# Performance work log

Hardware: AMD Instinct MI355X
Metric: run time of the kernel (lower is better)

The kernel has to match this reference:

```python
import jax, jax.numpy as jnp
import numpy as np

EDGE_TEXT_IMG = 2
D_MODEL = 256
N_HEADS = 8
N_LAYERS = 3
INPUT_DIM = 768
LN_EPS = 1e-5
CONFLICT_EPS = 1e-6


def setup_inputs() -> dict:
    key = jax.random.key(0)
    ks = jax.random.split(key, 32)
    B, N, E = 16, 512, 4096
    d, H, L = D_MODEL, N_HEADS, N_LAYERS
    s = 0.02
    inp = {
        'node_feats': jax.random.normal(ks[0], (B, N, INPUT_DIM), jnp.float32),
        'node_mask': jnp.ones((B, N), bool),
        'text_mask': jax.random.randint(ks[1], (B, N), 0, 2).astype(bool),
        'image_mask': jax.random.randint(ks[2], (B, N), 0, 2).astype(bool),
        'global_indices': jax.random.randint(ks[3], (B,), 0, N),
        'edge_index': jax.random.randint(ks[4], (B, 2, E), 0, N),
        'edge_type': jax.random.randint(ks[5], (B, E), 0, 4),
        'edge_weight': jax.random.uniform(ks[6], (B, E), jnp.float32),
        # params
        'W_in': jax.random.normal(ks[7], (INPUT_DIM, d)) * s,
        'b_in': jnp.zeros((d,)),
        'Wqkv': jax.random.normal(ks[8], (L, d, 3 * d)) * s,
        'bqkv': jnp.zeros((L, 3 * d)),
        'Wo': jax.random.normal(ks[9], (L, d, d)) * s,
        'bo': jnp.zeros((L, d)),
        'ln1_g': jnp.ones((L, d)), 'ln1_b': jnp.zeros((L, d)),
        'ln2_g': jnp.ones((L, d)), 'ln2_b': jnp.zeros((L, d)),
        'Wff1': jax.random.normal(ks[10], (L, d, 4 * d)) * s,
        'bff1': jnp.zeros((L, 4 * d)),
        'Wff2': jax.random.normal(ks[11], (L, 4 * d, d)) * s,
        'bff2': jnp.zeros((L, d)),
        'et_emb': jax.random.normal(ks[12], (4, H)) * s,
        'Wm1': jax.random.normal(ks[13], (3 * d + 1, 2 * d)) * s,
        'bm1': jnp.zeros((2 * d,)),
        'Wm2': jax.random.normal(ks[14], (2 * d, d)) * s,
        'bm2': jnp.zeros((d,)),
        'Wm3': jax.random.normal(ks[15], (d, 1)) * s,
        'bm3': jnp.zeros((1,)),
    }
    return inp


def _ln(x, g, b):
    mu = jnp.mean(x, -1, keepdims=True)
    var = jnp.mean((x - mu) ** 2, -1, keepdims=True)
    return (x - mu) * jax.lax.rsqrt(var + LN_EPS) * g + b


def _build_bias(edge_index, edge_type, edge_weight, et_emb, N):
    # vectorized scatter-add of per-edge head biases into dense [B,H,N,N]
    B = edge_index.shape[0]
    src, dst = edge_index[:, 0], edge_index[:, 1]  # [B,E]
    vals = et_emb[edge_type]  # [B,E,H]
    vals = vals + jnp.where(edge_type == EDGE_TEXT_IMG, edge_weight, 0.0)[..., None]
    bias = jnp.zeros((B, N, N, et_emb.shape[1]), vals.dtype)
    bias = bias.at[jnp.arange(B)[:, None], src, dst].add(vals)
    return bias.transpose(0, 3, 1, 2)  # [B,H,N,N]


def _forward(node_feats, node_mask, text_mask, image_mask, global_indices,
             edge_index, edge_type, edge_weight,
             W_in, b_in, Wqkv, bqkv, Wo, bo, ln1_g, ln1_b, ln2_g, ln2_b,
             Wff1, bff1, Wff2, bff2, et_emb, Wm1, bm1, Wm2, bm2, Wm3, bm3):
    B, N, _ = node_feats.shape
    H = N_HEADS
    hd = D_MODEL // H
    attn_bias = _build_bias(edge_index, edge_type, edge_weight, et_emb, N)
    x = node_feats @ W_in + b_in  # [B,N,d]
    key_mask = node_mask[:, None, None, :]  # [B,1,1,N]
    for l in range(N_LAYERS):
        qkv = x @ Wqkv[l] + bqkv[l]
        qkv = qkv.reshape(B, N, 3, H, hd).transpose(2, 0, 3, 1, 4)
        q, k, v = qkv[0], qkv[1], qkv[2]  # [B,H,N,hd]
        scores = jnp.einsum('bhnd,bhmd->bhnm', q, k) / np.sqrt(hd).astype(np.float32)
        scores = scores + attn_bias
        scores = jnp.where(key_mask, scores, -jnp.inf)
        attn = jax.nn.softmax(scores, axis=-1)
        out = jnp.einsum('bhnm,bhmd->bhnd', attn, v)
        out = out.transpose(0, 2, 1, 3).reshape(B, N, D_MODEL)
        out = out @ Wo[l] + bo[l]
        x = _ln(x + out, ln1_g[l], ln1_b[l])
        ff = jax.nn.gelu(x @ Wff1[l] + bff1[l], approximate=False) @ Wff2[l] + bff2[l]
        x = _ln(x + ff, ln2_g[l], ln2_b[l])
    tm = text_mask.astype(x.dtype)
    im = image_mask.astype(x.dtype)
    tc = jnp.clip(tm.sum(1, keepdims=True), 1.0)
    ic = jnp.clip(im.sum(1, keepdims=True), 1.0)
    text_pool = (x * tm[..., None]).sum(1) / tc
    image_pool = (x * im[..., None]).sum(1) / ic
    global_embeds = x[jnp.arange(B), global_indices]
    n1 = jnp.maximum(jnp.linalg.norm(text_pool, axis=-1), CONFLICT_EPS)
    n2 = jnp.maximum(jnp.linalg.norm(image_pool, axis=-1), CONFLICT_EPS)
    cos = jnp.sum(text_pool * image_pool, -1) / (n1 * n2)
    conflict = (1.0 - cos)[:, None]
    combined = jnp.concatenate([global_embeds, text_pool, image_pool, conflict], -1)
    h = jax.nn.gelu(combined @ Wm1 + bm1, approximate=False)
    h = jax.nn.gelu(h @ Wm2 + bm2, approximate=False)
    logits = (h @ Wm3 + bm3)[:, 0]
    return logits


def reference(node_feats, node_mask, text_mask, image_mask, global_indices,
              edge_index, edge_type, edge_weight,
              W_in, b_in, Wqkv, bqkv, Wo, bo, ln1_g, ln1_b, ln2_g, ln2_b,
              Wff1, bff1, Wff2, bff2, et_emb, Wm1, bm1, Wm2, bm2, Wm3, bm3):
    return _forward(node_feats, node_mask, text_mask, image_mask, global_indices,
                    edge_index, edge_type, edge_weight,
                    W_in, b_in, Wqkv, bqkv, Wo, bo, ln1_g, ln1_b, ln2_g, ln2_b,
                    Wff1, bff1, Wff2, bff2, et_emb, Wm1, bm1, Wm2, bm2, Wm3, bm3)
```

## Files before the change

kernel.cpp:

```cpp
#include <hip/hip_runtime.h>
#include <hip/hip_bf16.h>
#include <math.h>

#define Bb 16
#define Nn 512
#define Dd 256
#define Hh 8
#define HD 32
#define Ll 3
#define INDIM 768
#define Ee 4096
#define FF 1024
#define KP2 72
#define NBUCK 32768

typedef unsigned short u16;
typedef __bf16 bf16x8 __attribute__((ext_vector_type(8)));
typedef float f32x4 __attribute__((ext_vector_type(4)));
typedef u16 us8 __attribute__((ext_vector_type(8)));
typedef u16 us4 __attribute__((ext_vector_type(4)));

__device__ __forceinline__ float gelu_exact(float x) {
    return 0.5f * x * (1.0f + erff(x * 0.70710678118654752f));
}

__device__ __forceinline__ u16 f2bf(float x) {
    union { __bf16 b; u16 u; } cv;
    cv.b = (__bf16)x;
    return cv.u;
}
__device__ __forceinline__ float bf2f(u16 h) {
    return __uint_as_float(((unsigned int)h) << 16);
}

__device__ __forceinline__ int ebucket(int b, int src, int dst) {
    return ((b * 32 + (src >> 4)) * 4 + (dst >> 7)) * 16 + (src & 15);
}


__global__ __launch_bounds__(256) void zero2_kernel(int* __restrict__ a, int na,
                                                    int* __restrict__ b, int nb) {
    int gid = blockIdx.x * 256 + threadIdx.x;
    if (gid < na) a[gid] = 0;
    else {
        int j = gid - na;
        if (j < nb) b[j] = 0;
    }
}

__global__ __launch_bounds__(256) void count_kernel(const int* __restrict__ edge_index,
                                                    int* __restrict__ counts) {
    int gid = blockIdx.x * 256 + threadIdx.x;
    int b = gid >> 12;
    int e = gid & (Ee - 1);
    int src = edge_index[b * 2 * Ee + e];
    int dst = edge_index[b * 2 * Ee + Ee + e];
    atomicAdd(&counts[ebucket(b, src, dst)], 1);
}

__global__ __launch_bounds__(1024) void scan_kernel(const int* __restrict__ counts,
                                                    int* __restrict__ offsets,
                                                    int* __restrict__ cursor) {
    __shared__ int ssum[1024];
    int t = threadIdx.x;
    int local[32];
    int s = 0;
#pragma unroll
    for (int i = 0; i < 32; i++) { local[i] = counts[t * 32 + i]; s += local[i]; }
    ssum[t] = s;
    __syncthreads();
    for (int off = 1; off < 1024; off *= 2) {
        __syncthreads();
        int v = (t >= off) ? ssum[t - off] : 0;
        __syncthreads();
        ssum[t] += v;
    }
    __syncthreads();
    int base = (t > 0) ? ssum[t - 1] : 0;
#pragma unroll
    for (int i = 0; i < 32; i++) {
        offsets[t * 32 + i] = base;
        cursor[t * 32 + i] = base;
        base += local[i];
    }
    if (t == 1023) offsets[NBUCK] = base;
}

__global__ __launch_bounds__(256) void scatter_kernel(const int* __restrict__ edge_index,
                                                      const int* __restrict__ edge_type,
                                                      const float* __restrict__ edge_weight,
                                                      int* __restrict__ cursor,
                                                      int2* __restrict__ pelist) {
    int gid = blockIdx.x * 256 + threadIdx.x;
    int b = gid >> 12;
    int e = gid & (Ee - 1);
    int src = edge_index[b * 2 * Ee + e];
    int dst = edge_index[b * 2 * Ee + Ee + e];
    int ty = edge_type[b * Ee + e];
    float wgt = edge_weight[b * Ee + e];
    int pos = atomicAdd(&cursor[ebucket(b, src, dst)], 1);
    int2 pe;
    pe.x = (src << 20) | (dst << 4) | ty;
    pe.y = __float_as_int(wgt);
    pelist[pos] = pe;
}


__global__ __launch_bounds__(256) void wsplit(const float* __restrict__ W,
                                              u16* __restrict__ Wh,
                                              u16* __restrict__ Wl,
                                              int K, int N) {
    size_t moff = (size_t)blockIdx.z * K * N;
    const float* Ws = W + moff;
    u16* Whs = Wh + moff;
    u16* Wls = Wl + moff;
    int n = blockIdx.x * 256 + threadIdx.x;
    int k0 = blockIdx.y * 8;
    float w[8];
#pragma unroll
    for (int i = 0; i < 8; i++) w[i] = Ws[(size_t)(k0 + i) * N + n];
    u16 h[8], l[8];
#pragma unroll
    for (int i = 0; i < 8; i++) {
        h[i] = f2bf(w[i]);
        l[i] = f2bf(w[i] - bf2f(h[i]));
    }
    us8 hv = {h[0], h[1], h[2], h[3], h[4], h[5], h[6], h[7]};
    us8 lv = {l[0], l[1], l[2], l[3], l[4], l[5], l[6], l[7]};
    *(us8*)&Whs[(size_t)n * K + k0] = hv;
    *(us8*)&Wls[(size_t)n * K + k0] = lv;
}


__global__ __launch_bounds__(256) void gemm_mfma64(const float* __restrict__ A,
                                                   const u16* __restrict__ Bh,
                                                   const u16* __restrict__ Bl,
                                                   const float* __restrict__ bias,
                                                   float* __restrict__ C,
                                                   int M, int K, int N, int act) {
    __shared__ u16 sAh[64 * KP2];
    __shared__ u16 sAl[64 * KP2];
    __shared__ u16 sBh[64 * KP2];
    __shared__ u16 sBl[64 * KP2];

    int t = threadIdx.x;
    int w = t >> 6, L = t & 63;
    int wr = w >> 1, wc = w & 1;
    int lane15 = L & 15, quad = L >> 4;
    int row0 = blockIdx.y * 64, col0 = blockIdx.x * 64;

    f32x4 acc[2][2];
#pragma unroll
    for (int mi = 0; mi < 2; mi++)
#pragma unroll
        for (int ni = 0; ni < 2; ni++) acc[mi][ni] = {0.f, 0.f, 0.f, 0.f};

    int ar0 = t >> 3, ak0 = (t & 7) * 8;
    int bn0 = t >> 2, bk0 = (t & 3) * 16;

    const float* Ap0 = &A[(size_t)(row0 + ar0) * K + ak0];
    const float* Ap1 = &A[(size_t)(row0 + ar0 + 32) * K + ak0];
    const u16* Bhp = &Bh[(size_t)(col0 + bn0) * K + bk0];
    const u16* Blp = &Bl[(size_t)(col0 + bn0) * K + bk0];

    float4 av0[2], av1[2];
    us8 bhv[2], blv[2];
#pragma unroll
    for (int j = 0; j < 2; j++) {
        av0[j] = *(const float4*)&Ap0[4 * j];
        av1[j] = *(const float4*)&Ap1[4 * j];
        bhv[j] = *(const us8*)&Bhp[8 * j];
        blv[j] = *(const us8*)&Blp[8 * j];
    }

    for (int k0 = 0; k0 < K; k0 += 64) {
        __syncthreads();
#pragma unroll
        for (int j = 0; j < 2; j++) {
            {
                float a[4] = {av0[j].x, av0[j].y, av0[j].z, av0[j].w};
                u16 h[4], l[4];
#pragma unroll
                for (int i = 0; i < 4; i++) { h[i] = f2bf(a[i]); l[i] = f2bf(a[i] - bf2f(h[i])); }
                us4 hv = {h[0], h[1], h[2], h[3]};
                us4 lv = {l[0], l[1], l[2], l[3]};
                *(us4*)&sAh[ar0 * KP2 + ak0 + 4 * j] = hv;
                *(us4*)&sAl[ar0 * KP2 + ak0 + 4 * j] = lv;
            }
            {
                float a[4] = {av1[j].x, av1[j].y, av1[j].z, av1[j].w};
                u16 h[4], l[4];
#pragma unroll
                for (int i = 0; i < 4; i++) { h[i] = f2bf(a[i]); l[i] = f2bf(a[i] - bf2f(h[i])); }
                us4 hv = {h[0], h[1], h[2], h[3]};
                us4 lv = {l[0], l[1], l[2], l[3]};
                *(us4*)&sAh[(ar0 + 32) * KP2 + ak0 + 4 * j] = hv;
                *(us4*)&sAl[(ar0 + 32) * KP2 + ak0 + 4 * j] = lv;
            }
            *(us8*)&sBh[bn0 * KP2 + bk0 + 8 * j] = bhv[j];
            *(us8*)&sBl[bn0 * KP2 + bk0 + 8 * j] = blv[j];
        }
        __syncthreads();

        if (k0 + 64 < K) {
#pragma unroll
            for (int j = 0; j < 2; j++) {
                av0[j] = *(const float4*)&Ap0[k0 + 64 + 4 * j];
                av1[j] = *(const float4*)&Ap1[k0 + 64 + 4 * j];
                bhv[j] = *(const us8*)&Bhp[k0 + 64 + 8 * j];
                blv[j] = *(const us8*)&Blp[k0 + 64 + 8 * j];
            }
        }

#pragma unroll
        for (int half = 0; half < 2; half++) {
            int kofs = half * 32 + quad * 8;
            us8 ahr[2], alr[2], bhr[2], blr[2];
#pragma unroll
            for (int mi = 0; mi < 2; mi++) {
                int ro = (wr * 32 + mi * 16 + lane15) * KP2 + kofs;
                ahr[mi] = *(const us8*)&sAh[ro];
                alr[mi] = *(const us8*)&sAl[ro];
            }
#pragma unroll
            for (int ni = 0; ni < 2; ni++) {
                int ro = (wc * 32 + ni * 16 + lane15) * KP2 + kofs;
                bhr[ni] = *(const us8*)&sBh[ro];
                blr[ni] = *(const us8*)&sBl[ro];
            }
#pragma unroll
            for (int mi = 0; mi < 2; mi++) {
                bf16x8 ah = *(const bf16x8*)&ahr[mi];
                bf16x8 al = *(const bf16x8*)&alr[mi];
#pragma unroll
                for (int ni = 0; ni < 2; ni++) {
                    bf16x8 bh = *(const bf16x8*)&bhr[ni];
                    bf16x8 bl = *(const bf16x8*)&blr[ni];
                    acc[mi][ni] = __builtin_amdgcn_mfma_f32_16x16x32_bf16(ah, bh, acc[mi][ni], 0, 0, 0);
                    acc[mi][ni] = __builtin_amdgcn_mfma_f32_16x16x32_bf16(ah, bl, acc[mi][ni], 0, 0, 0);
                    acc[mi][ni] = __builtin_amdgcn_mfma_f32_16x16x32_bf16(al, bh, acc[mi][ni], 0, 0, 0);
                }
            }
        }
    }

#pragma unroll
    for (int mi = 0; mi < 2; mi++) {
#pragma unroll
        for (int ni = 0; ni < 2; ni++) {
            int col = col0 + wc * 32 + ni * 16 + lane15;
            float bcol = bias[col];
#pragma unroll
            for (int r = 0; r < 4; r++) {
                int row = row0 + wr * 32 + mi * 16 + quad * 4 + r;
                float u = acc[mi][ni][r] + bcol;
                if (act == 1) u = gelu_exact(u);
                C[(size_t)row * N + col] = u;
            }
        }
    }
}


__global__ __launch_bounds__(256) void gemm_mfma128(const float* __restrict__ A,
                                                    const u16* __restrict__ Bh,
                                                    const u16* __restrict__ Bl,
                                                    const float* __restrict__ bias,
                                                    float* __restrict__ C,
                                                    int M, int K, int N, int act) {
    __shared__ u16 sAh[128 * KP2];
    __shared__ u16 sAl[128 * KP2];
    __shared__ u16 sBh[128 * KP2];
    __shared__ u16 sBl[128 * KP2];

    int t = threadIdx.x;
    int w = t >> 6, L = t & 63;
    int wr = w >> 1, wc = w & 1;
    int lane15 = L & 15, quad = L >> 4;
    int row0 = blockIdx.y * 128, col0 = blockIdx.x * 128;

    f32x4 acc[4][4];
#pragma unroll
    for (int mi = 0; mi < 4; mi++)
#pragma unroll
        for (int ni = 0; ni < 4; ni++) acc[mi][ni] = {0.f, 0.f, 0.f, 0.f};

    int ar0 = t >> 3, ak0 = (t & 7) * 8;
    int bn0 = t >> 2, bk0 = (t & 3) * 16;

    const float* Ap = &A[(size_t)(row0 + ar0) * K + ak0];
    const u16* Bhp = &Bh[(size_t)(col0 + bn0) * K + bk0];
    const u16* Blp = &Bl[(size_t)(col0 + bn0) * K + bk0];

    float4 av[4][2];
    us8 bhv[2][2], blv[2][2];
#pragma unroll
    for (int i = 0; i < 4; i++)
#pragma unroll
        for (int j = 0; j < 2; j++) av[i][j] = *(const float4*)&Ap[(size_t)(32 * i) * K + 4 * j];
#pragma unroll
    for (int i = 0; i < 2; i++)
#pragma unroll
        for (int j = 0; j < 2; j++) {
            bhv[i][j] = *(const us8*)&Bhp[(size_t)(64 * i) * K + 8 * j];
            blv[i][j] = *(const us8*)&Blp[(size_t)(64 * i) * K + 8 * j];
        }

    for (int k0 = 0; k0 < K; k0 += 64) {
        __syncthreads();
#pragma unroll
        for (int i = 0; i < 4; i++)
#pragma unroll
            for (int j = 0; j < 2; j++) {
                float a[4] = {av[i][j].x, av[i][j].y, av[i][j].z, av[i][j].w};
                u16 h[4], l[4];
#pragma unroll
                for (int q = 0; q < 4; q++) { h[q] = f2bf(a[q]); l[q] = f2bf(a[q] - bf2f(h[q])); }
                us4 hv = {h[0], h[1], h[2], h[3]};
                us4 lv = {l[0], l[1], l[2], l[3]};
                *(us4*)&sAh[(ar0 + 32 * i) * KP2 + ak0 + 4 * j] = hv;
                *(us4*)&sAl[(ar0 + 32 * i) * KP2 + ak0 + 4 * j] = lv;
            }
#pragma unroll
        for (int i = 0; i < 2; i++)
#pragma unroll
            for (int j = 0; j < 2; j++) {
                *(us8*)&sBh[(bn0 + 64 * i) * KP2 + bk0 + 8 * j] = bhv[i][j];
                *(us8*)&sBl[(bn0 + 64 * i) * KP2 + bk0 + 8 * j] = blv[i][j];
            }
        __syncthreads();

        if (k0 + 64 < K) {
#pragma unroll
            for (int i = 0; i < 4; i++)
#pragma unroll
                for (int j = 0; j < 2; j++)
                    av[i][j] = *(const float4*)&Ap[(size_t)(32 * i) * K + k0 + 64 + 4 * j];
#pragma unroll
            for (int i = 0; i < 2; i++)
#pragma unroll
                for (int j = 0; j < 2; j++) {
                    bhv[i][j] = *(const us8*)&Bhp[(size_t)(64 * i) * K + k0 + 64 + 8 * j];
                    blv[i][j] = *(const us8*)&Blp[(size_t)(64 * i) * K + k0 + 64 + 8 * j];
                }
        }

#pragma unroll
        for (int half = 0; half < 2; half++) {
            int kofs = half * 32 + quad * 8;
            us8 ahr[4], alr[4], bhr[4], blr[4];
#pragma unroll
            for (int mi = 0; mi < 4; mi++) {
                int ro = (wr * 64 + mi * 16 + lane15) * KP2 + kofs;
                ahr[mi] = *(const us8*)&sAh[ro];
                alr[mi] = *(const us8*)&sAl[ro];
            }
#pragma unroll
            for (int ni = 0; ni < 4; ni++) {
                int ro = (wc * 64 + ni * 16 + lane15) * KP2 + kofs;
                bhr[ni] = *(const us8*)&sBh[ro];
                blr[ni] = *(const us8*)&sBl[ro];
            }
#pragma unroll
            for (int mi = 0; mi < 4; mi++) {
                bf16x8 ah = *(const bf16x8*)&ahr[mi];
                bf16x8 al = *(const bf16x8*)&alr[mi];
#pragma unroll
                for (int ni = 0; ni < 4; ni++) {
                    bf16x8 bh = *(const bf16x8*)&bhr[ni];
                    bf16x8 bl = *(const bf16x8*)&blr[ni];
                    acc[mi][ni] = __builtin_amdgcn_mfma_f32_16x16x32_bf16(ah, bh, acc[mi][ni], 0, 0, 0);
                    acc[mi][ni] = __builtin_amdgcn_mfma_f32_16x16x32_bf16(ah, bl, acc[mi][ni], 0, 0, 0);
                    acc[mi][ni] = __builtin_amdgcn_mfma_f32_16x16x32_bf16(al, bh, acc[mi][ni], 0, 0, 0);
                }
            }
        }
    }

#pragma unroll
    for (int mi = 0; mi < 4; mi++) {
#pragma unroll
        for (int ni = 0; ni < 4; ni++) {
            int col = col0 + wc * 64 + ni * 16 + lane15;
            float bcol = bias[col];
#pragma unroll
            for (int r = 0; r < 4; r++) {
                int row = row0 + wr * 64 + mi * 16 + quad * 4 + r;
                float u = acc[mi][ni][r] + bcol;
                if (act == 1) u = gelu_exact(u);
                C[(size_t)row * N + col] = u;
            }
        }
    }
}


#define SBP 132

__global__ __launch_bounds__(256, 2) void attn_kernel(const float* __restrict__ qkv,
                                                      const int* __restrict__ node_mask,
                                                      const int* __restrict__ offsets,
                                                      const int2* __restrict__ pelist,
                                                      const float* __restrict__ et_emb,
                                                      float* __restrict__ outbuf) {
    int bid = blockIdx.x;
    int quarter = bid & 3;
    int h = (bid >> 2) & 7;
    int b = bid >> 5;
    int t = threadIdx.x;
    int w = t >> 6, L = t & 63;
    int quad = L >> 4, lane15 = L & 15;
    int q8 = quad * 8;

    __shared__ u16 sKh[128 * 40];
    __shared__ u16 sKl[128 * 40];
    __shared__ u16 sVh[32 * SBP];
    __shared__ u16 sVl[32 * SBP];
    __shared__ float sS[4 * 16 * SBP];

    float* Sw = &sS[w * 16 * SBP];
    const float scale = 0.17677669529663687f;
    int nbase = quarter * 128 + w * 32;
    int mt0 = t >> 5, dt = t & 31;

    float etl0 = et_emb[0 * Hh + h];
    float etl1 = et_emb[1 * Hh + h];
    float etl2 = et_emb[2 * Hh + h];
    float etl3 = et_emb[3 * Hh + h];

    us8 Qh[2], Ql[2];
#pragma unroll
    for (int sub = 0; sub < 2; sub++) {
        size_t row = (size_t)(b * Nn + nbase + sub * 16 + lane15);
        float4 qa = *(const float4*)&qkv[row * 768 + h * HD + q8];
        float4 qb = *(const float4*)&qkv[row * 768 + h * HD + q8 + 4];
        float qv[8] = {qa.x, qa.y, qa.z, qa.w, qb.x, qb.y, qb.z, qb.w};
#pragma unroll
        for (int j = 0; j < 8; j++) {
            float xq = qv[j] * scale;
            u16 hh = f2bf(xq);
            Qh[sub][j] = hh;
            Ql[sub][j] = f2bf(xq - bf2f(hh));
        }
    }

    float Mst[2] = {-INFINITY, -INFINITY};
    float Lst[2] = {0.0f, 0.0f};
    f32x4 O[2][2];
#pragma unroll
    for (int sub = 0; sub < 2; sub++)
#pragma unroll
        for (int dc = 0; dc < 2; dc++) O[sub][dc] = {0.f, 0.f, 0.f, 0.f};

    float pk[16], pv[16];
#pragma unroll
    for (int j = 0; j < 16; j++) {
        size_t grow = (size_t)(b * Nn + mt0 + 8 * j) * 768 + h * HD + dt;
        pk[j] = qkv[grow + 256];
        pv[j] = qkv[grow + 512];
    }

    for (int T = 0; T < 4; T++) {
        int m0 = T * 128;
        __syncthreads();
#pragma unroll
        for (int j = 0; j < 16; j++) {
            int m = mt0 + 8 * j;
            u16 kh = f2bf(pk[j]);
            sKh[m * 40 + dt] = kh;
            sKl[m * 40 + dt] = f2bf(pk[j] - bf2f(kh));
            u16 vh = f2bf(pv[j]);
            sVh[dt * SBP + m] = vh;
            sVl[dt * SBP + m] = f2bf(pv[j] - bf2f(vh));
        }
        __syncthreads();
        if (T < 3) {
#pragma unroll
            for (int j = 0; j < 16; j++) {
                size_t grow = (size_t)(b * Nn + (T + 1) * 128 + mt0 + 8 * j) * 768 + h * HD + dt;
                pk[j] = qkv[grow + 256];
                pv[j] = qkv[grow + 512];
            }
        }

        float mk[4][8];
#pragma unroll
        for (int c = 0; c < 4; c++) {
            int4 u0 = *(const int4*)&node_mask[b * Nn + m0 + c * 32 + q8];
            int4 u1 = *(const int4*)&node_mask[b * Nn + m0 + c * 32 + q8 + 4];
            mk[c][0] = u0.x ? 0.f : -INFINITY;
            mk[c][1] = u0.y ? 0.f : -INFINITY;
            mk[c][2] = u0.z ? 0.f : -INFINITY;
            mk[c][3] = u0.w ? 0.f : -INFINITY;
            mk[c][4] = u1.x ? 0.f : -INFINITY;
            mk[c][5] = u1.y ? 0.f : -INFINITY;
            mk[c][6] = u1.z ? 0.f : -INFINITY;
            mk[c][7] = u1.w ? 0.f : -INFINITY;
        }

#pragma unroll
        for (int sub = 0; sub < 2; sub++) {
            int nsub = nbase + sub * 16;
            bf16x8 qh = *(const bf16x8*)&Qh[sub];
            bf16x8 ql = *(const bf16x8*)&Ql[sub];

            f32x4 accS[8];
#pragma unroll
            for (int mc = 0; mc < 8; mc++) accS[mc] = {0.f, 0.f, 0.f, 0.f};
#pragma unroll
            for (int mc = 0; mc < 8; mc++) {
                us8 khr = *(const us8*)&sKh[(mc * 16 + lane15) * 40 + q8];
                us8 klr = *(const us8*)&sKl[(mc * 16 + lane15) * 40 + q8];
                bf16x8 kh = *(const bf16x8*)&khr;
                bf16x8 kl = *(const bf16x8*)&klr;
                accS[mc] = __builtin_amdgcn_mfma_f32_16x16x32_bf16(qh, kh, accS[mc], 0, 0, 0);
                accS[mc] = __builtin_amdgcn_mfma_f32_16x16x32_bf16(qh, kl, accS[mc], 0, 0, 0);
                accS[mc] = __builtin_amdgcn_mfma_f32_16x16x32_bf16(ql, kh, accS[mc], 0, 0, 0);
            }
#pragma unroll
            for (int mc = 0; mc < 8; mc++)
#pragma unroll
                for (int r = 0; r < 4; r++)
                    Sw[(quad * 4 + r) * SBP + mc * 16 + lane15] = accS[mc][r];
            asm volatile("s_waitcnt lgkmcnt(0)" ::: "memory");

            int gb = ((b * 32 + (nsub >> 4)) * 4 + T) * 16;
            int beg = offsets[gb];
// ... 81 lines not shown
#pragma unroll
    for (int sub = 0; sub < 2; sub++) {
        float linv = 1.0f / Lst[sub];
        float lD[4];
#pragma unroll
        for (int r = 0; r < 4; r++) lD[r] = __shfl(linv, (L & 48) | (quad * 4 + r));
#pragma unroll
        for (int dc = 0; dc < 2; dc++)
#pragma unroll
            for (int r = 0; r < 4; r++) {
                int row = nbase + sub * 16 + quad * 4 + r;
                outbuf[(size_t)(b * Nn + row) * Dd + h * HD + dc * 16 + lane15] =
                    O[sub][dc][r] * lD[r];
            }
    }
}


__global__ __launch_bounds__(256) void ln_kernel(float* __restrict__ x,
                                                 const float* __restrict__ res,
                                                 const float* __restrict__ g,
                                                 const float* __restrict__ bta) {
    int row = blockIdx.x * 4 + (threadIdx.x >> 6);
    int L = threadIdx.x & 63;
    size_t base = (size_t)row * Dd + L * 4;
    float4 v4 = *(const float4*)&x[base];
    float4 r4 = *(const float4*)&res[base];
    float v0 = v4.x + r4.x, v1 = v4.y + r4.y, v2 = v4.z + r4.z, v3 = v4.w + r4.w;
    float sm = v0 + v1 + v2 + v3;
#pragma unroll
    for (int o = 32; o > 0; o >>= 1) sm += __shfl_xor(sm, o);
    float mu = sm * (1.0f / Dd);
    float d0 = v0 - mu, d1 = v1 - mu, d2 = v2 - mu, d3 = v3 - mu;
    float s2 = d0 * d0 + d1 * d1 + d2 * d2 + d3 * d3;
#pragma unroll
    for (int o = 32; o > 0; o >>= 1) s2 += __shfl_xor(s2, o);
    float rsig = 1.0f / sqrtf(s2 * (1.0f / Dd) + 1e-5f);
    float4 g4 = *(const float4*)&g[L * 4];
    float4 b4 = *(const float4*)&bta[L * 4];
    float4 o4;
    o4.x = d0 * rsig * g4.x + b4.x;
    o4.y = d1 * rsig * g4.y + b4.y;
    o4.z = d2 * rsig * g4.z + b4.z;
    o4.w = d3 * rsig * g4.w + b4.w;
    *(float4*)&x[base] = o4;
}


__global__ __launch_bounds__(256) void pool_kernel(const float* __restrict__ x,
                                                   const int* __restrict__ text_mask,
                                                   const int* __restrict__ image_mask,
                                                   float* __restrict__ pools) {
    int b = blockIdx.y;
    int n0 = blockIdx.x * 32;
    int t = threadIdx.x;
    float tp = 0.0f, ip = 0.0f, c1 = 0.0f, c2 = 0.0f;
    for (int n = n0; n < n0 + 32; n++) {
        float xv = x[(size_t)(b * Nn + n) * Dd + t];
        int tm = text_mask[b * Nn + n];
        int im = image_mask[b * Nn + n];
        tp += tm ? xv : 0.0f;
        ip += im ? xv : 0.0f;
        c1 += (float)tm;
        c2 += (float)im;
    }
    atomicAdd(&pools[b * 514 + t], tp);
    atomicAdd(&pools[b * 514 + 256 + t], ip);
    if (t == 0) {
        atomicAdd(&pools[b * 514 + 512], c1);
        atomicAdd(&pools[b * 514 + 513], c2);
    }
}

__global__ __launch_bounds__(256) void comb_kernel(const float* __restrict__ x,
                                                   const float* __restrict__ pools,
                                                   const int* __restrict__ gidx,
                                                   float* __restrict__ comb) {
    int b = blockIdx.x;
    int t = threadIdx.x;
    __shared__ float redd[12];
    float tc = fmaxf(pools[b * 514 + 512], 1.0f);
    float ic = fmaxf(pools[b * 514 + 513], 1.0f);
    float tp = pools[b * 514 + t] / tc;
    float ip = pools[b * 514 + 256 + t] / ic;
    int gi = gidx[b];
    comb[b * 776 + t] = x[(size_t)(b * Nn + gi) * Dd + t];
    comb[b * 776 + 256 + t] = tp;
    comb[b * 776 + 512 + t] = ip;
    float dotv = tp * ip, n1v = tp * tp, n2v = ip * ip;
    for (int o = 32; o > 0; o >>= 1) {
        dotv += __shfl_down(dotv, o);
        n1v += __shfl_down(n1v, o);
        n2v += __shfl_down(n2v, o);
    }
    if ((t & 63) == 0) { redd[t >> 6] = dotv; redd[4 + (t >> 6)] = n1v; redd[8 + (t >> 6)] = n2v; }
    __syncthreads();
    if (t == 0) {
        float dd = redd[0] + redd[1] + redd[2] + redd[3];
        float a1 = fmaxf(sqrtf(redd[4] + redd[5] + redd[6] + redd[7]), 1e-6f);
        float a2 = fmaxf(sqrtf(redd[8] + redd[9] + redd[10] + redd[11]), 1e-6f);
        comb[b * 776 + 768] = 1.0f - dd / (a1 * a2);
    }
}

__global__ __launch_bounds__(256) void h1_kernel(const float* __restrict__ comb,
                                                 const float* __restrict__ Wm1,
                                                 const float* __restrict__ bm1,
                                                 float* __restrict__ h1) {
    int b = blockIdx.y;
    int jc = blockIdx.x;
    int t = threadIdx.x;
    __shared__ float scomb[776];
    __shared__ float partial[2][128];
    for (int i = t; i < 769; i += 256) scomb[i] = comb[b * 776 + i];
    __syncthreads();
    int j = jc * 128 + (t & 127);
    int kh = t >> 7;
    int kbeg = kh ? 384 : 0;
    int kend = kh ? 769 : 384;
    float acc = 0.0f;
#pragma unroll 8
    for (int k = kbeg; k < kend; k++) acc += scomb[k] * Wm1[k * 512 + j];
    partial[kh][t & 127] = acc;
    __syncthreads();
    if (t < 128) {
        float v = partial[0][t] + partial[1][t] + bm1[jc * 128 + t];
        h1[b * 512 + jc * 128 + t] = gelu_exact(v);
    }
}

__global__ __launch_bounds__(256) void head_fin(const float* __restrict__ h1,
                                                const float* __restrict__ Wm2,
                                                const float* __restrict__ bm2,
                                                const float* __restrict__ Wm3,
                                                const float* __restrict__ bm3,
                                                float* __restrict__ out) {
    int b = blockIdx.x;
    int t = threadIdx.x;
    __shared__ float h1s[512];
    __shared__ float red[4];
    for (int i = t; i < 512; i += 256) h1s[i] = h1[b * 512 + i];
    __syncthreads();
    float acc = bm2[t];
#pragma unroll 8
    for (int k = 0; k < 512; k++) acc += h1s[k] * Wm2[k * 256 + t];
    float h2 = gelu_exact(acc);
    float lv = h2 * Wm3[t];
    for (int o = 32; o > 0; o >>= 1) lv += __shfl_down(lv, o);
    if ((t & 63) == 0) red[t >> 6] = lv;
    __syncthreads();
    if (t == 0) out[b] = red[0] + red[1] + red[2] + red[3] + bm3[0];
}


#define OFF_IN  0
#define OFF_QKV 196608
#define OFF_O   786432
#define OFF_F1  983040
#define OFF_F2  1769472
#define W_TOTAL 2555904

extern "C" void kernel_launch(void* const* d_in, const int* in_sizes, int n_in,
                              void* d_out, int out_size, void* d_ws, size_t ws_size,
                              hipStream_t stream) {
    const float* node_feats = (const float*)d_in[0];
    const int* node_mask = (const int*)d_in[1];
    const int* text_mask = (const int*)d_in[2];
    const int* image_mask = (const int*)d_in[3];
    const int* gidx = (const int*)d_in[4];
    const int* edge_index = (const int*)d_in[5];
    const int* edge_type = (const int*)d_in[6];
    const float* edge_weight = (const float*)d_in[7];
    const float* W_in = (const float*)d_in[8];
    const float* b_in = (const float*)d_in[9];
    const float* Wqkv = (const float*)d_in[10];
    const float* bqkv = (const float*)d_in[11];
    const float* Wo = (const float*)d_in[12];
    const float* bo = (const float*)d_in[13];
    const float* ln1_g = (const float*)d_in[14];
    const float* ln1_b = (const float*)d_in[15];
    const float* ln2_g = (const float*)d_in[16];
    const float* ln2_b = (const float*)d_in[17];
    const float* Wff1 = (const float*)d_in[18];
    const float* bff1 = (const float*)d_in[19];
    const float* Wff2 = (const float*)d_in[20];
    const float* bff2 = (const float*)d_in[21];
    const float* et_emb = (const float*)d_in[22];
    const float* Wm1 = (const float*)d_in[23];
    const float* bm1 = (const float*)d_in[24];
    const float* Wm2 = (const float*)d_in[25];
    const float* bm2 = (const float*)d_in[26];
    const float* Wm3 = (const float*)d_in[27];
    const float* bm3 = (const float*)d_in[28];

    const int M = Bb * Nn;
    char* ws = (char*)d_ws;
    size_t off = 0;
    auto alloc = [&](size_t bytes) {
        void* p = ws + off;
        off += (bytes + 255) & ~(size_t)255;
        return p;
    };
    float* x = (float*)alloc((size_t)M * Dd * 4);
    float* qkvb = (float*)alloc((size_t)M * FF * 4);
    float* ffb = qkvb;
    float* attnout = (float*)alloc((size_t)M * Dd * 4);
    float* projb = (float*)alloc((size_t)M * Dd * 4);
    int* counts = (int*)alloc((size_t)NBUCK * 4);
    int* offsets = (int*)alloc((size_t)(NBUCK + 1) * 4);
    int* cursor = (int*)alloc((size_t)NBUCK * 4);
    int2* pelist = (int2*)alloc((size_t)Bb * Ee * 8);
    float* pools = (float*)alloc((size_t)Bb * 514 * 4);
    float* comb = (float*)alloc((size_t)Bb * 776 * 4);
    float* h1 = (float*)alloc((size_t)Bb * 512 * 4);
    u16* wh = (u16*)alloc((size_t)W_TOTAL * 2);
    u16* wl = (u16*)alloc((size_t)W_TOTAL * 2);
    (void)ws_size;

    zero2_kernel<<<(NBUCK + Bb * 514 + 255) / 256, 256, 0, stream>>>(
        counts, NBUCK, (int*)pools, Bb * 514);
    count_kernel<<<256, 256, 0, stream>>>(edge_index, counts);
    scan_kernel<<<1, 1024, 0, stream>>>(counts, offsets, cursor);
    scatter_kernel<<<256, 256, 0, stream>>>(edge_index, edge_type, edge_weight, cursor, pelist);

    wsplit<<<dim3(1, 96, 1), 256, 0, stream>>>(W_in, wh + OFF_IN, wl + OFF_IN, 768, 256);
    wsplit<<<dim3(3, 32, 3), 256, 0, stream>>>(Wqkv, wh + OFF_QKV, wl + OFF_QKV, 256, 768);
    wsplit<<<dim3(1, 32, 3), 256, 0, stream>>>(Wo, wh + OFF_O, wl + OFF_O, 256, 256);
    wsplit<<<dim3(4, 32, 3), 256, 0, stream>>>(Wff1, wh + OFF_F1, wl + OFF_F1, 256, 1024);
    wsplit<<<dim3(1, 128, 3), 256, 0, stream>>>(Wff2, wh + OFF_F2, wl + OFF_F2, 1024, 256);

    gemm_mfma64<<<dim3(Dd / 64, M / 64), 256, 0, stream>>>(
        node_feats, wh + OFF_IN, wl + OFF_IN, b_in, x, M, INDIM, Dd, 0);

    for (int l = 0; l < Ll; l++) {
        gemm_mfma128<<<dim3(768 / 128, M / 128), 256, 0, stream>>>(
            x, wh + OFF_QKV + (size_t)l * 196608, wl + OFF_QKV + (size_t)l * 196608,
            bqkv + l * 768, qkvb, M, Dd, 768, 0);
        attn_kernel<<<Bb * Hh * 4, 256, 0, stream>>>(
            qkvb, node_mask, offsets, pelist, et_emb, attnout);
        gemm_mfma64<<<dim3(Dd / 64, M / 64), 256, 0, stream>>>(
            attnout, wh + OFF_O + (size_t)l * 65536, wl + OFF_O + (size_t)l * 65536,
            bo + l * Dd, projb, M, Dd, Dd, 0);
        ln_kernel<<<M / 4, 256, 0, stream>>>(x, projb, ln1_g + l * Dd, ln1_b + l * Dd);
        gemm_mfma128<<<dim3(FF / 128, M / 128), 256, 0, stream>>>(
            x, wh + OFF_F1 + (size_t)l * 262144, wl + OFF_F1 + (size_t)l * 262144,
            bff1 + l * FF, ffb, M, Dd, FF, 1);
        gemm_mfma64<<<dim3(Dd / 64, M / 64), 256, 0, stream>>>(
            ffb, wh + OFF_F2 + (size_t)l * 262144, wl + OFF_F2 + (size_t)l * 262144,
            bff2 + l * Dd, projb, M, FF, Dd, 0);
        ln_kernel<<<M / 4, 256, 0, stream>>>(x, projb, ln2_g + l * Dd, ln2_b + l * Dd);
    }

    pool_kernel<<<dim3(16, Bb), 256, 0, stream>>>(x, text_mask, image_mask, pools);
    comb_kernel<<<Bb, 256, 0, stream>>>(x, pools, gidx, comb);
    h1_kernel<<<dim3(4, Bb), 256, 0, stream>>>(comb, Wm1, bm1, h1);
    head_fin<<<Bb, 256, 0, stream>>>(h1, Wm2, bm2, Wm3, bm3, (float*)d_out);
}
```

Before: 620.4 us.

## Double-buffer GEMM shared memory with smaller K tiles and merge weight-split launches

Both MFMA GEMM kernels now use a K tile of 32 instead of 64 and two shared-memory buffers. This removes one barrier per iteration and lets stores for the next tile overlap the MFMA work on the current one. Launch bounds now request two blocks per CU to raise occupancy. The five weight hi/lo split kernels are merged into one launch to cut launch overhead. In exchange, each K step does less work, so there are more loop iterations, and the row padding of 36 elements may change LDS bank-conflict behaviour.

```diff
diff --git a/kernel.cpp b/kernel.cpp
--- a/kernel.cpp
+++ b/kernel.cpp
@@ -11,7 +11,7 @@
 #define INDIM 768
 #define Ee 4096
 #define FF 1024
-#define KP2 72
+#define KP3 36
 #define NBUCK 32768
 
 typedef unsigned short u16;
@@ -106,19 +106,57 @@
 }
 
 
-__global__ __launch_bounds__(256) void wsplit(const float* __restrict__ W,
-                                              u16* __restrict__ Wh,
-                                              u16* __restrict__ Wl,
-                                              int K, int N) {
-    size_t moff = (size_t)blockIdx.z * K * N;
-    const float* Ws = W + moff;
-    u16* Whs = Wh + moff;
-    u16* Wls = Wl + moff;
-    int n = blockIdx.x * 256 + threadIdx.x;
-    int k0 = blockIdx.y * 8;
+#define OFF_IN  0
+#define OFF_QKV 196608
+#define OFF_O   786432
+#define OFF_F1  983040
+#define OFF_F2  1769472
+#define W_TOTAL 2555904
+
+__global__ __launch_bounds__(256) void wsplit_all(const float* __restrict__ W_in,
+                                                  const float* __restrict__ Wqkv,
+                                                  const float* __restrict__ Wo,
+                                                  const float* __restrict__ Wff1,
+                                                  const float* __restrict__ Wff2,
+                                                  u16* __restrict__ wh,
+                                                  u16* __restrict__ wl) {
+    int bid = blockIdx.x;
+    const float* W;
+    u16 *Wh, *Wl;
+    int K, N, nb, kb;
+    if (bid < 96) {
+        W = W_in; Wh = wh + OFF_IN; Wl = wl + OFF_IN;
+        K = 768; N = 256; nb = 0; kb = bid;
+    } else if (bid < 384) {
+        int lb = bid - 96; int l = lb / 96; lb -= l * 96;
+        W = Wqkv + (size_t)l * 196608;
+        Wh = wh + OFF_QKV + (size_t)l * 196608;
+        Wl = wl + OFF_QKV + (size_t)l * 196608;
+        K = 256; N = 768; nb = lb % 3; kb = lb / 3;
+    } else if (bid < 480) {
+        int lb = bid - 384; int l = lb / 32; lb -= l * 32;
+        W = Wo + (size_t)l * 65536;
+        Wh = wh + OFF_O + (size_t)l * 65536;
+        Wl = wl + OFF_O + (size_t)l * 65536;
+        K = 256; N = 256; nb = 0; kb = lb;
+    } else if (bid < 864) {
+        int lb = bid - 480; int l = lb / 128; lb -= l * 128;
+        W = Wff1 + (size_t)l * 262144;
+        Wh = wh + OFF_F1 + (size_t)l * 262144;
+        Wl = wl + OFF_F1 + (size_t)l * 262144;
+        K = 256; N = 1024; nb = lb % 4; kb = lb / 4;
+    } else {
+        int lb = bid - 864; int l = lb / 128; lb -= l * 128;
+        W = Wff2 + (size_t)l * 262144;
+        Wh = wh + OFF_F2 + (size_t)l * 262144;
+        Wl = wl + OFF_F2 + (size_t)l * 262144;
+        K = 1024; N = 256; nb = 0; kb = lb;
+    }
+    int n = nb * 256 + threadIdx.x;
+    int k0 = kb * 8;
     float w[8];
 #pragma unroll
-    for (int i = 0; i < 8; i++) w[i] = Ws[(size_t)(k0 + i) * N + n];
+    for (int i = 0; i < 8; i++) w[i] = W[(size_t)(k0 + i) * N + n];
     u16 h[8], l[8];
 #pragma unroll
     for (int i = 0; i < 8; i++) {
@@ -127,21 +165,21 @@
     }
     us8 hv = {h[0], h[1], h[2], h[3], h[4], h[5], h[6], h[7]};
     us8 lv = {l[0], l[1], l[2], l[3], l[4], l[5], l[6], l[7]};
-    *(us8*)&Whs[(size_t)n * K + k0] = hv;
-    *(us8*)&Wls[(size_t)n * K + k0] = lv;
-}
-
-
-__global__ __launch_bounds__(256) void gemm_mfma64(const float* __restrict__ A,
-                                                   const u16* __restrict__ Bh,
-                                                   const u16* __restrict__ Bl,
-                                                   const float* __restrict__ bias,
-                                                   float* __restrict__ C,
-                                                   int M, int K, int N, int act) {
-    __shared__ u16 sAh[64 * KP2];
-    __shared__ u16 sAl[64 * KP2];
-    __shared__ u16 sBh[64 * KP2];
-    __shared__ u16 sBl[64 * KP2];
+    *(us8*)&Wh[(size_t)n * K + k0] = hv;
+    *(us8*)&Wl[(size_t)n * K + k0] = lv;
+}
+
+
+__global__ __launch_bounds__(256, 2) void gemm_mfma64(const float* __restrict__ A,
+                                                      const u16* __restrict__ Bh,
+                                                      const u16* __restrict__ Bl,
+                                                      const float* __restrict__ bias,
+                                                      float* __restrict__ C,
+                                                      int M, int K, int N, int act) {
+    __shared__ u16 sAh[2][64 * KP3];
+    __shared__ u16 sAl[2][64 * KP3];
+    __shared__ u16 sBh[2][64 * KP3];
+    __shared__ u16 sBl[2][64 * KP3];
 
     int t = threadIdx.x;
     int w = t >> 6, L = t & 63;
@@ -155,91 +193,103 @@
 #pragma unroll
         for (int ni = 0; ni < 2; ni++) acc[mi][ni] = {0.f, 0.f, 0.f, 0.f};
 
-    int ar0 = t >> 3, ak0 = (t & 7) * 8;
-    int bn0 = t >> 2, bk0 = (t & 3) * 16;
+    int ar0 = t >> 3, ak0 = (t & 7) * 4;
+    int bn0 = t >> 2, bk0 = (t & 3) * 8;
 
     const float* Ap0 = &A[(size_t)(row0 + ar0) * K + ak0];
     const float* Ap1 = &A[(size_t)(row0 + ar0 + 32) * K + ak0];
     const u16* Bhp = &Bh[(size_t)(col0 + bn0) * K + bk0];
     const u16* Blp = &Bl[(size_t)(col0 + bn0) * K + bk0];
 
-    float4 av0[2], av1[2];
-    us8 bhv[2], blv[2];
-#pragma unroll
-    for (int j = 0; j < 2; j++) {
-        av0[j] = *(const float4*)&Ap0[4 * j];
-        av1[j] = *(const float4*)&Ap1[4 * j];
-        bhv[j] = *(const us8*)&Bhp[8 * j];
-        blv[j] = *(const us8*)&Blp[8 * j];
-    }
-
-    for (int k0 = 0; k0 < K; k0 += 64) {
+    float4 av0, av1;
+    us8 bhv, blv;
+    av0 = *(const float4*)&Ap0[0];
+    av1 = *(const float4*)&Ap1[0];
+    bhv = *(const us8*)&Bhp[0];
+    blv = *(const us8*)&Blp[0];
+
+    int nit = K >> 5;
+
+    {
+        float a0[4] = {av0.x, av0.y, av0.z, av0.w};
+        float a1[4] = {av1.x, av1.y, av1.z, av1.w};
+        u16 h0[4], l0[4], h1[4], l1[4];
+#pragma unroll
+        for (int i = 0; i < 4; i++) {
+            h0[i] = f2bf(a0[i]); l0[i] = f2bf(a0[i] - bf2f(h0[i]));
+            h1[i] = f2bf(a1[i]); l1[i] = f2bf(a1[i] - bf2f(h1[i]));
+        }
+        us4 hv0 = {h0[0], h0[1], h0[2], h0[3]}, lv0 = {l0[0], l0[1], l0[2], l0[3]};
+        us4 hv1 = {h1[0], h1[1], h1[2], h1[3]}, lv1 = {l1[0], l1[1], l1[2], l1[3]};
+        *(us4*)&sAh[0][ar0 * KP3 + ak0] = hv0;
+        *(us4*)&sAl[0][ar0 * KP3 + ak0] = lv0;
+        *(us4*)&sAh[0][(ar0 + 32) * KP3 + ak0] = hv1;
+        *(us4*)&sAl[0][(ar0 + 32) * KP3 + ak0] = lv1;
+        *(us8*)&sBh[0][bn0 * KP3 + bk0] = bhv;
+        *(us8*)&sBl[0][bn0 * KP3 + bk0] = blv;
+    }
+    if (nit > 1) {
+        av0 = *(const float4*)&Ap0[32];
+        av1 = *(const float4*)&Ap1[32];
+        bhv = *(const us8*)&Bhp[32];
+        blv = *(const us8*)&Blp[32];
+    }
+
+    for (int i = 0; i < nit; i++) {
         __syncthreads();
-#pragma unroll
-        for (int j = 0; j < 2; j++) {
-            {
-                float a[4] = {av0[j].x, av0[j].y, av0[j].z, av0[j].w};
-                u16 h[4], l[4];
-#pragma unroll
-                for (int i = 0; i < 4; i++) { h[i] = f2bf(a[i]); l[i] = f2bf(a[i] - bf2f(h[i])); }
-                us4 hv = {h[0], h[1], h[2], h[3]};
-                us4 lv = {l[0], l[1], l[2], l[3]};
-                *(us4*)&sAh[ar0 * KP2 + ak0 + 4 * j] = hv;
-                *(us4*)&sAl[ar0 * KP2 + ak0 + 4 * j] = lv;
-            }
-            {
-                float a[4] = {av1[j].x, av1[j].y, av1[j].z, av1[j].w};
-                u16 h[4], l[4];
-#pragma unroll
-                for (int i = 0; i < 4; i++) { h[i] = f2bf(a[i]); l[i] = f2bf(a[i] - bf2f(h[i])); }
-                us4 hv = {h[0], h[1], h[2], h[3]};
-                us4 lv = {l[0], l[1], l[2], l[3]};
-                *(us4*)&sAh[(ar0 + 32) * KP2 + ak0 + 4 * j] = hv;
-                *(us4*)&sAl[(ar0 + 32) * KP2 + ak0 + 4 * j] = lv;
-            }
-            *(us8*)&sBh[bn0 * KP2 + bk0 + 8 * j] = bhv[j];
-            *(us8*)&sBl[bn0 * KP2 + bk0 + 8 * j] = blv[j];
-        }
-        __syncthreads();
-
-        if (k0 + 64 < K) {
-#pragma unroll
-            for (int j = 0; j < 2; j++) {
-                av0[j] = *(const float4*)&Ap0[k0 + 64 + 4 * j];
-                av1[j] = *(const float4*)&Ap1[k0 + 64 + 4 * j];
-                bhv[j] = *(const us8*)&Bhp[k0 + 64 + 8 * j];
-                blv[j] = *(const us8*)&Blp[k0 + 64 + 8 * j];
-            }
-        }
-
-#pragma unroll
-        for (int half = 0; half < 2; half++) {
-            int kofs = half * 32 + quad * 8;
-            us8 ahr[2], alr[2], bhr[2], blr[2];
-#pragma unroll
-            for (int mi = 0; mi < 2; mi++) {
-                int ro = (wr * 32 + mi * 16 + lane15) * KP2 + kofs;
-                ahr[mi] = *(const us8*)&sAh[ro];
-                alr[mi] = *(const us8*)&sAl[ro];
-            }
+        int cur = i & 1;
+        if (i + 1 < nit) {
+            int nxt = cur ^ 1;
+            float a0[4] = {av0.x, av0.y, av0.z, av0.w};
+            float a1[4] = {av1.x, av1.y, av1.z, av1.w};
+            u16 h0[4], l0[4], h1[4], l1[4];
+#pragma unroll
+            for (int q = 0; q < 4; q++) {
+                h0[q] = f2bf(a0[q]); l0[q] = f2bf(a0[q] - bf2f(h0[q]));
+                h1[q] = f2bf(a1[q]); l1[q] = f2bf(a1[q] - bf2f(h1[q]));
+            }
+            us4 hv0 = {h0[0], h0[1], h0[2], h0[3]}, lv0 = {l0[0], l0[1], l0[2], l0[3]};
+            us4 hv1 = {h1[0], h1[1], h1[2], h1[3]}, lv1 = {l1[0], l1[1], l1[2], l1[3]};
+            *(us4*)&sAh[nxt][ar0 * KP3 + ak0] = hv0;
+            *(us4*)&sAl[nxt][ar0 * KP3 + ak0] = lv0;
+            *(us4*)&sAh[nxt][(ar0 + 32) * KP3 + ak0] = hv1;
+            *(us4*)&sAl[nxt][(ar0 + 32) * KP3 + ak0] = lv1;
+            *(us8*)&sBh[nxt][bn0 * KP3 + bk0] = bhv;
+            *(us8*)&sBl[nxt][bn0 * KP3 + bk0] = blv;
+            if (i + 2 < nit) {
+                int ko = (i + 2) * 32;
+                av0 = *(const float4*)&Ap0[ko];
+                av1 = *(const float4*)&Ap1[ko];
+                bhv = *(const us8*)&Bhp[ko];
+                blv = *(const us8*)&Blp[ko];
+            }
+        }
+
+        int kof = quad * 8;
+        us8 ahr[2], alr[2], bhr[2], blr[2];
+#pragma unroll
+        for (int mi = 0; mi < 2; mi++) {
+            int ro = (wr * 32 + mi * 16 + lane15) * KP3 + kof;
+            ahr[mi] = *(const us8*)&sAh[cur][ro];
+            alr[mi] = *(const us8*)&sAl[cur][ro];
+        }
+#pragma unroll
+        for (int ni = 0; ni < 2; ni++) {
+            int ro = (wc * 32 + ni * 16 + lane15) * KP3 + kof;
+            bhr[ni] = *(const us8*)&sBh[cur][ro];
+            blr[ni] = *(const us8*)&sBl[cur][ro];
+        }
+#pragma unroll
+        for (int mi = 0; mi < 2; mi++) {
+            bf16x8 ah = *(const bf16x8*)&ahr[mi];
+            bf16x8 al = *(const bf16x8*)&alr[mi];
 #pragma unroll
             for (int ni = 0; ni < 2; ni++) {
-                int ro = (wc * 32 + ni * 16 + lane15) * KP2 + kofs;
-                bhr[ni] = *(const us8*)&sBh[ro];
-                blr[ni] = *(const us8*)&sBl[ro];
-            }
-#pragma unroll
-            for (int mi = 0; mi < 2; mi++) {
-                bf16x8 ah = *(const bf16x8*)&ahr[mi];
-                bf16x8 al = *(const bf16x8*)&alr[mi];
-#pragma unroll
-                for (int ni = 0; ni < 2; ni++) {
-                    bf16x8 bh = *(const bf16x8*)&bhr[ni];
-                    bf16x8 bl = *(const bf16x8*)&blr[ni];
-                    acc[mi][ni] = __builtin_amdgcn_mfma_f32_16x16x32_bf16(ah, bh, acc[mi][ni], 0, 0, 0);
-                    acc[mi][ni] = __builtin_amdgcn_mfma_f32_16x16x32_bf16(ah, bl, acc[mi][ni], 0, 0, 0);
-                    acc[mi][ni] = __builtin_amdgcn_mfma_f32_16x16x32_bf16(al, bh, acc[mi][ni], 0, 0, 0);
-                }
+                bf16x8 bh = *(const bf16x8*)&bhr[ni];
+                bf16x8 bl = *(const bf16x8*)&blr[ni];
+                acc[mi][ni] = __builtin_amdgcn_mfma_f32_16x16x32_bf16(ah, bh, acc[mi][ni], 0, 0, 0);
+                acc[mi][ni] = __builtin_amdgcn_mfma_f32_16x16x32_bf16(ah, bl, acc[mi][ni], 0, 0, 0);
+                acc[mi][ni] = __builtin_amdgcn_mfma_f32_16x16x32_bf16(al, bh, acc[mi][ni], 0, 0, 0);
             }
         }
     }
@@ -262,16 +312,16 @@
 }
 
 
-__global__ __launch_bounds__(256) void gemm_mfma128(const float* __restrict__ A,
-                                                    const u16* __restrict__ Bh,
-                                                    const u16* __restrict__ Bl,
-                                                    const float* __restrict__ bias,
-                                                    float* __restrict__ C,
-                                                    int M, int K, int N, int act) {
-    __shared__ u16 sAh[128 * KP2];
-    __shared__ u16 sAl[128 * KP2];
-    __shared__ u16 sBh[128 * KP2];
-    __shared__ u16 sBl[128 * KP2];
+__global__ __launch_bounds__(256, 2) void gemm_mfma128(const float* __restrict__ A,
+                                                       const u16* __restrict__ Bh,
+                                                       const u16* __restrict__ Bl,
+                                                       const float* __restrict__ bias,
+                                                       float* __restrict__ C,
+                                                       int M, int K, int N, int act) {
+    __shared__ u16 sAh[2][128 * KP3];
+    __shared__ u16 sAl[2][128 * KP3];
+    __shared__ u16 sBh[2][128 * KP3];
+    __shared__ u16 sBl[2][128 * KP3];
 
     int t = threadIdx.x;
     int w = t >> 6, L = t & 63;
@@ -285,94 +335,109 @@
 #pragma unroll
         for (int ni = 0; ni < 4; ni++) acc[mi][ni] = {0.f, 0.f, 0.f, 0.f};
 
-    int ar0 = t >> 3, ak0 = (t & 7) * 8;
-    int bn0 = t >> 2, bk0 = (t & 3) * 16;
+    int ar0 = t >> 3, ak0 = (t & 7) * 4;
+    int bn0 = t >> 2, bk0 = (t & 3) * 8;
 
     const float* Ap = &A[(size_t)(row0 + ar0) * K + ak0];
     const u16* Bhp = &Bh[(size_t)(col0 + bn0) * K + bk0];
     const u16* Blp = &Bl[(size_t)(col0 + bn0) * K + bk0];
 
-    float4 av[4][2];
-    us8 bhv[2][2], blv[2][2];
-#pragma unroll
-    for (int i = 0; i < 4; i++)
-#pragma unroll
-        for (int j = 0; j < 2; j++) av[i][j] = *(const float4*)&Ap[(size_t)(32 * i) * K + 4 * j];
-#pragma unroll
-    for (int i = 0; i < 2; i++)
-#pragma unroll
-        for (int j = 0; j < 2; j++) {
-            bhv[i][j] = *(const us8*)&Bhp[(size_t)(64 * i) * K + 8 * j];
-            blv[i][j] = *(const us8*)&Blp[(size_t)(64 * i) * K + 8 * j];
-        }
-
-    for (int k0 = 0; k0 < K; k0 += 64) {
+    float4 av[4];
+    us8 bhv[2], blv[2];
+#pragma unroll
+    for (int i = 0; i < 4; i++) av[i] = *(const float4*)&Ap[(size_t)(32 * i) * K];
+#pragma unroll
+    for (int i = 0; i < 2; i++) {
+        bhv[i] = *(const us8*)&Bhp[(size_t)(64 * i) * K];
+        blv[i] = *(const us8*)&Blp[(size_t)(64 * i) * K];
+    }
+
+    int nit = K >> 5;
+
+#pragma unroll
+    for (int i = 0; i < 4; i++) {
+        float a[4] = {av[i].x, av[i].y, av[i].z, av[i].w};
+        u16 h[4], l[4];
+#pragma unroll
+        for (int q = 0; q < 4; q++) { h[q] = f2bf(a[q]); l[q] = f2bf(a[q] - bf2f(h[q])); }
+        us4 hv = {h[0], h[1], h[2], h[3]};
+        us4 lv = {l[0], l[1], l[2], l[3]};
+        *(us4*)&sAh[0][(ar0 + 32 * i) * KP3 + ak0] = hv;
+        *(us4*)&sAl[0][(ar0 + 32 * i) * KP3 + ak0] = lv;
+    }
+#pragma unroll
+    for (int i = 0; i < 2; i++) {
+        *(us8*)&sBh[0][(bn0 + 64 * i) * KP3 + bk0] = bhv[i];
+        *(us8*)&sBl[0][(bn0 + 64 * i) * KP3 + bk0] = blv[i];
+    }
+    if (nit > 1) {
+#pragma unroll
+        for (int i = 0; i < 4; i++) av[i] = *(const float4*)&Ap[(size_t)(32 * i) * K + 32];
+#pragma unroll
+        for (int i = 0; i < 2; i++) {
+            bhv[i] = *(const us8*)&Bhp[(size_t)(64 * i) * K + 32];
+            blv[i] = *(const us8*)&Blp[(size_t)(64 * i) * K + 32];
+        }
+    }
+
+    for (int it = 0; it < nit; it++) {
         __syncthreads();
-#pragma unroll
-        for (int i = 0; i < 4; i++)
-#pragma unroll
-            for (int j = 0; j < 2; j++) {
-                float a[4] = {av[i][j].x, av[i][j].y, av[i][j].z, av[i][j].w};
+        int cur = it & 1;
+        if (it + 1 < nit) {
+            int nxt = cur ^ 1;
+#pragma unroll
+            for (int i = 0; i < 4; i++) {
+                float a[4] = {av[i].x, av[i].y, av[i].z, av[i].w};
                 u16 h[4], l[4];
 #pragma unroll
                 for (int q = 0; q < 4; q++) { h[q] = f2bf(a[q]); l[q] = f2bf(a[q] - bf2f(h[q])); }
                 us4 hv = {h[0], h[1], h[2], h[3]};
                 us4 lv = {l[0], l[1], l[2], l[3]};
-                *(us4*)&sAh[(ar0 + 32 * i) * KP2 + ak0 + 4 * j] = hv;
-                *(us4*)&sAl[(ar0 + 32 * i) * KP2 + ak0 + 4 * j] = lv;
-            }
-#pragma unroll
-        for (int i = 0; i < 2; i++)
-#pragma unroll
-            for (int j = 0; j < 2; j++) {
-                *(us8*)&sBh[(bn0 + 64 * i) * KP2 + bk0 + 8 * j] = bhv[i][j];
-                *(us8*)&sBl[(bn0 + 64 * i) * KP2 + bk0 + 8 * j] = blv[i][j];
-            }
-        __syncthreads();
-
-        if (k0 + 64 < K) {
-#pragma unroll
-            for (int i = 0; i < 4; i++)
-#pragma unroll
-                for (int j = 0; j < 2; j++)
-                    av[i][j] = *(const float4*)&Ap[(size_t)(32 * i) * K + k0 + 64 + 4 * j];
-#pragma unroll
-            for (int i = 0; i < 2; i++)
-#pragma unroll
-                for (int j = 0; j < 2; j++) {
-                    bhv[i][j] = *(const us8*)&Bhp[(size_t)(64 * i) * K + k0 + 64 + 8 * j];
-                    blv[i][j] = *(const us8*)&Blp[(size_t)(64 * i) * K + k0 + 64 + 8 * j];
+                *(us4*)&sAh[nxt][(ar0 + 32 * i) * KP3 + ak0] = hv;
+                *(us4*)&sAl[nxt][(ar0 + 32 * i) * KP3 + ak0] = lv;
+            }
+#pragma unroll
+            for (int i = 0; i < 2; i++) {
+                *(us8*)&sBh[nxt][(bn0 + 64 * i) * KP3 + bk0] = bhv[i];
+                *(us8*)&sBl[nxt][(bn0 + 64 * i) * KP3 + bk0] = blv[i];
+            }
+            if (it + 2 < nit) {
+                int ko = (it + 2) * 32;
+#pragma unroll
+                for (int i = 0; i < 4; i++) av[i] = *(const float4*)&Ap[(size_t)(32 * i) * K + ko];
+#pragma unroll
+                for (int i = 0; i < 2; i++) {
+                    bhv[i] = *(const us8*)&Bhp[(size_t)(64 * i) * K + ko];
+                    blv[i] = *(const us8*)&Blp[(size_t)(64 * i) * K + ko];
                 }
-        }
-
-#pragma unroll
-        for (int half = 0; half < 2; half++) {
-            int kofs = half * 32 + quad * 8;
-            us8 ahr[4], alr[4], bhr[4], blr[4];
-#pragma unroll
-            for (int mi = 0; mi < 4; mi++) {
-                int ro = (wr * 64 + mi * 16 + lane15) * KP2 + kofs;
-                ahr[mi] = *(const us8*)&sAh[ro];
-                alr[mi] = *(const us8*)&sAl[ro];
-            }
+            }
+        }
+
+        int kof = quad * 8;
+        us8 ahr[4], alr[4], bhr[4], blr[4];
+#pragma unroll
+        for (int mi = 0; mi < 4; mi++) {
+            int ro = (wr * 64 + mi * 16 + lane15) * KP3 + kof;
+            ahr[mi] = *(const us8*)&sAh[cur][ro];
+            alr[mi] = *(const us8*)&sAl[cur][ro];
+        }
+#pragma unroll
+        for (int ni = 0; ni < 4; ni++) {
+            int ro = (wc * 64 + ni * 16 + lane15) * KP3 + kof;
+            bhr[ni] = *(const us8*)&sBh[cur][ro];
+            blr[ni] = *(const us8*)&sBl[cur][ro];
+        }
+#pragma unroll
+        for (int mi = 0; mi < 4; mi++) {
+            bf16x8 ah = *(const bf16x8*)&ahr[mi];
+            bf16x8 al = *(const bf16x8*)&alr[mi];
 #pragma unroll
             for (int ni = 0; ni < 4; ni++) {
-                int ro = (wc * 64 + ni * 16 + lane15) * KP2 + kofs;
-                bhr[ni] = *(const us8*)&sBh[ro];
-                blr[ni] = *(const us8*)&sBl[ro];
-            }
-#pragma unroll
-            for (int mi = 0; mi < 4; mi++) {
-                bf16x8 ah = *(const bf16x8*)&ahr[mi];
-                bf16x8 al = *(const bf16x8*)&alr[mi];
-#pragma unroll
-                for (int ni = 0; ni < 4; ni++) {
-                    bf16x8 bh = *(const bf16x8*)&bhr[ni];
-                    bf16x8 bl = *(const bf16x8*)&blr[ni];
-                    acc[mi][ni] = __builtin_amdgcn_mfma_f32_16x16x32_bf16(ah, bh, acc[mi][ni], 0, 0, 0);
-                    acc[mi][ni] = __builtin_amdgcn_mfma_f32_16x16x32_bf16(ah, bl, acc[mi][ni], 0, 0, 0);
-                    acc[mi][ni] = __builtin_amdgcn_mfma_f32_16x16x32_bf16(al, bh, acc[mi][ni], 0, 0, 0);
-                }
+                bf16x8 bh = *(const bf16x8*)&bhr[ni];
+                bf16x8 bl = *(const bf16x8*)&blr[ni];
+                acc[mi][ni] = __builtin_amdgcn_mfma_f32_16x16x32_bf16(ah, bh, acc[mi][ni], 0, 0, 0);
+                acc[mi][ni] = __builtin_amdgcn_mfma_f32_16x16x32_bf16(ah, bl, acc[mi][ni], 0, 0, 0);
+                acc[mi][ni] = __builtin_amdgcn_mfma_f32_16x16x32_bf16(al, bh, acc[mi][ni], 0, 0, 0);
             }
         }
     }
@@ -760,13 +825,6 @@
     if (t == 0) out[b] = red[0] + red[1] + red[2] + red[3] + bm3[0];
 }
 
-
-#define OFF_IN  0
-#define OFF_QKV 196608
-#define OFF_O   786432
-#define OFF_F1  983040
-#define OFF_F2  1769472
-#define W_TOTAL 2555904
 
 extern "C" void kernel_launch(void* const* d_in, const int* in_sizes, int n_in,
                               void* d_out, int out_size, void* d_ws, size_t ws_size,
@@ -831,11 +889,7 @@
     scan_kernel<<<1, 1024, 0, stream>>>(counts, offsets, cursor);
     scatter_kernel<<<256, 256, 0, stream>>>(edge_index, edge_type, edge_weight, cursor, pelist);
 
-    wsplit<<<dim3(1, 96, 1), 256, 0, stream>>>(W_in, wh + OFF_IN, wl + OFF_IN, 768, 256);
-    wsplit<<<dim3(3, 32, 3), 256, 0, stream>>>(Wqkv, wh + OFF_QKV, wl + OFF_QKV, 256, 768);
-    wsplit<<<dim3(1, 32, 3), 256, 0, stream>>>(Wo, wh + OFF_O, wl + OFF_O, 256, 256);
-    wsplit<<<dim3(4, 32, 3), 256, 0, stream>>>(Wff1, wh + OFF_F1, wl + OFF_F1, 256, 1024);
-    wsplit<<<dim3(1, 128, 3), 256, 0, stream>>>(Wff2, wh + OFF_F2, wl + OFF_F2, 1024, 256);
+    wsplit_all<<<1248, 256, 0, stream>>>(W_in, Wqkv, Wo, Wff1, Wff2, wh, wl);
 
     gemm_mfma64<<<dim3(Dd / 64, M / 64), 256, 0, stream>>>(
         node_feats, wh + OFF_IN, wl + OFF_IN, b_in, x, M, INDIM, Dd, 0);
```

Result: faster. 604.0 us (-2.6%).
